# Kernel tuning notes

Measured on AMD Instinct MI355X. Metric: run time of the kernel, lower is better.

The kernel has to match this reference:

```python
import jax, jax.numpy as jnp
import numpy as np
import math

B, S, D = 1, 2048, 2048          # batch, seq_len, hidden_size
H, HD = 16, 128                  # attention heads, head_dim
HV, R, NV, K = 4, 128, 2048, 4   # inner value heads, retrieval dim, num_inner_values, values per head


def rotate_half(x):
    x1, x2 = x[..., :x.shape[-1] // 2], x[..., x.shape[-1] // 2:]
    return jnp.concatenate((-x2, x1), axis=-1)


def setup_inputs() -> dict:
    key = jax.random.key(0)
    ks = jax.random.split(key, 8)
    hidden_states = jax.random.normal(ks[0], (B, S, D), jnp.float32)
    attention_mask = jnp.ones((B, S), jnp.float32)
    # standard RoPE tables, shape [B, S, HD]
    inv_freq = 1.0 / (10000.0 ** (jnp.arange(0, HD, 2, dtype=jnp.float32) / HD))
    freqs = jnp.outer(jnp.arange(S, dtype=jnp.float32), inv_freq)
    emb = jnp.concatenate((freqs, freqs), axis=-1)
    cos = jnp.broadcast_to(jnp.cos(emb)[None], (B, S, HD))
    sin = jnp.broadcast_to(jnp.sin(emb)[None], (B, S, HD))
    # learned per-head dynamic mask (binary, like torch.round init)
    dynamic_mask = jnp.round(jax.random.uniform(ks[1], (H, S), jnp.float32))
    sc = 0.02
    Wq = jax.random.normal(ks[2], (D, D), jnp.float32) * sc
    Wk = jax.random.normal(ks[3], (D, D), jnp.float32) * sc
    Wvq = jax.random.normal(ks[4], (D, HV * R), jnp.float32) * sc
    v_keys = jax.random.normal(ks[5], (HV, R, NV), jnp.float32) * sc
    v_embed = jax.random.normal(ks[6], (NV, D), jnp.float32) * sc
    Wo = jax.random.normal(ks[7], (D, D), jnp.float32) * sc
    return dict(hidden_states=hidden_states, attention_mask=attention_mask,
                cos=cos, sin=sin, dynamic_mask=dynamic_mask,
                Wq=Wq, Wk=Wk, Wvq=Wvq, v_keys=v_keys, v_embed=v_embed, Wo=Wo)


def reference(hidden_states, attention_mask, cos, sin, dynamic_mask,
              Wq, Wk, Wvq, v_keys, v_embed, Wo):
    b, s, d = hidden_states.shape
    q = hidden_states @ Wq
    k = hidden_states @ Wk
    # ---- inner_func: product-key style value retrieval ----
    vq = (hidden_states @ Wvq).reshape(b, s, HV, R).transpose(0, 2, 1, 3)  # [b,HV,s,R]
    sim = jnp.einsum('bhsr,hrn->bhsn', vq, v_keys)                         # [b,HV,s,NV]
    _, idx = jax.lax.top_k(sim, K)                                         # [b,HV,s,K]
    ve = v_embed[idx]                                                      # [b,HV,s,K,d]
    v = hidden_states * ve.sum(axis=3).sum(axis=1)                         # [b,s,d]
    # ---- heads ----
    q = q.reshape(b, s, H, HD).transpose(0, 2, 1, 3)
    k = k.reshape(b, s, H, HD).transpose(0, 2, 1, 3)
    v = v.reshape(b, s, H, HD).transpose(0, 2, 1, 3)
    # NOTE: original code rotates ONLY q (k is never rotated) -- kept faithfully
    cu, su = cos[:, None], sin[:, None]                                    # [b,1,s,HD]
    q = q * cu + rotate_half(q) * su
    attn = jnp.einsum('bhqd,bhkd->bhqk', q, k) / math.sqrt(HD)
    # ---- causal mask fused with per-head dynamic mask ----
    min_v = jnp.finfo(attn.dtype).min
    i = jnp.arange(s)
    causal = jnp.where(i[None, :] > i[:, None], min_v, 0.0).astype(attn.dtype)   # [s,s]
    causal = jnp.broadcast_to(causal[None, None], (b, H, s, s))
    am = attention_mask[:, None, None, :] * dynamic_mask[None, :, None, :s]      # [b,H,1,s]
    mask = jnp.where(causal + am == 0, min_v, causal)
    p = jax.nn.softmax(attn + mask, axis=-1)
    out = jnp.einsum('bhqk,bhkd->bhqd', p, v)
    out = out.transpose(0, 2, 1, 3).reshape(b, s, d)
    return out @ Wo
```

## Files before the change

kernel.cpp:

```cpp
#include <hip/hip_runtime.h>
#include <float.h>

#define NEG_MIN (-3.4028234663852886e38f)
#define INV_SQRT_HD 0.08838834764831845f
#define SCALE_L2E 0.12751791437968458f

typedef __attribute__((ext_vector_type(8))) short bf16x8;
typedef __attribute__((ext_vector_type(8))) unsigned short u16x8;
typedef __attribute__((ext_vector_type(4))) float f32x4;

__device__ __forceinline__ void gload_lds16(const void* g, void* l) {
  __builtin_amdgcn_global_load_lds((const __attribute__((address_space(1))) void*)g,
                                   (__attribute__((address_space(3))) void*)l, 16, 0, 0);
}
__device__ __forceinline__ ushort f2bf(float x) {
  union { float f; unsigned u; } v; v.f = x;
  unsigned r = v.u + 0x7fffu + ((v.u >> 16) & 1u);
  return (ushort)(r >> 16);
}
__device__ __forceinline__ float bf2f(ushort u) {
  union { unsigned i; float f; } v; v.i = ((unsigned)u) << 16; return v.f;
}
template<int CTRL>
__device__ __forceinline__ float dpp_ror(float x) {
  return __int_as_float(__builtin_amdgcn_mov_dpp(__float_as_int(x), CTRL, 0xF, 0xF, true));
}
template<int CTRL>
__device__ __forceinline__ unsigned dpp_ror_u(unsigned x) {
  return (unsigned)__builtin_amdgcn_mov_dpp((int)x, CTRL, 0xF, 0xF, true);
}
__device__ __forceinline__ unsigned wave_umax64(unsigned x) {
  x = max(x, dpp_ror_u<0x121>(x));
  x = max(x, dpp_ror_u<0x122>(x));
  x = max(x, dpp_ror_u<0x124>(x));
  x = max(x, dpp_ror_u<0x128>(x));
  x = max(x, (unsigned)__shfl_xor((int)x, 16));
  x = max(x, (unsigned)__shfl_xor((int)x, 32));
  return x;
}
__device__ __forceinline__ unsigned bf_sortable(ushort b) {
  return (b & 0x8000u) ? (unsigned)(b ^ 0xFFFFu) : (unsigned)(b | 0x8000u);
}

__global__ __launch_bounds__(256) void gemm_f32_sk(
    const float* __restrict__ A, int lda,
    const float* __restrict__ B, int ldb,
    float* __restrict__ Cp, int ldc, int M, int N, int Kchunk)
{
  __shared__ float As[16][132];
  __shared__ float Bs[16][132];
  const int t = threadIdx.x, tx = t & 15, ty = t >> 4;
  const int bm = blockIdx.y << 7, bn = blockIdx.x << 7;
  const int k0base = blockIdx.z * Kchunk;
  const int arr = t >> 2, ac = (t & 3) << 2;
  const int brr = t >> 5, bc = (t & 31) << 2;

  float acc[8][8];
#pragma unroll
  for (int i = 0; i < 8; ++i)
#pragma unroll
    for (int j = 0; j < 8; ++j) acc[i][j] = 0.f;

  float4 pa0, pa1, pb0, pb1;
  pa0 = *(const float4*)(A + (size_t)(bm + arr) * lda + k0base + ac);
  pa1 = *(const float4*)(A + (size_t)(bm + arr + 64) * lda + k0base + ac);
  pb0 = *(const float4*)(B + (size_t)(k0base + brr) * ldb + bn + bc);
  pb1 = *(const float4*)(B + (size_t)(k0base + brr + 8) * ldb + bn + bc);

  for (int k0 = 0; k0 < Kchunk; k0 += 16) {
    __syncthreads();
    As[ac + 0][arr] = pa0.x; As[ac + 1][arr] = pa0.y;
    As[ac + 2][arr] = pa0.z; As[ac + 3][arr] = pa0.w;
    As[ac + 0][arr + 64] = pa1.x; As[ac + 1][arr + 64] = pa1.y;
    As[ac + 2][arr + 64] = pa1.z; As[ac + 3][arr + 64] = pa1.w;
    *(float4*)(&Bs[brr][bc])     = pb0;
    *(float4*)(&Bs[brr + 8][bc]) = pb1;
    __syncthreads();
    if (k0 + 16 < Kchunk) {
      int kn = k0base + k0 + 16;
      pa0 = *(const float4*)(A + (size_t)(bm + arr) * lda + kn + ac);
      pa1 = *(const float4*)(A + (size_t)(bm + arr + 64) * lda + kn + ac);
      pb0 = *(const float4*)(B + (size_t)(kn + brr) * ldb + bn + bc);
      pb1 = *(const float4*)(B + (size_t)(kn + brr + 8) * ldb + bn + bc);
    }
#pragma unroll
    for (int kk = 0; kk < 16; ++kk) {
      float4 a0 = *(const float4*)(&As[kk][ty * 8]);
      float4 a1 = *(const float4*)(&As[kk][ty * 8 + 4]);
      float4 b0 = *(const float4*)(&Bs[kk][tx * 4]);
      float4 b1 = *(const float4*)(&Bs[kk][tx * 4 + 64]);
      float av[8] = {a0.x, a0.y, a0.z, a0.w, a1.x, a1.y, a1.z, a1.w};
      float bv[8] = {b0.x, b0.y, b0.z, b0.w, b1.x, b1.y, b1.z, b1.w};
#pragma unroll
      for (int i = 0; i < 8; ++i)
#pragma unroll
        for (int j = 0; j < 8; ++j)
          acc[i][j] = fmaf(av[i], bv[j], acc[i][j]);
    }
  }
  float* C = Cp + (size_t)blockIdx.z * M * N;
#pragma unroll
  for (int i = 0; i < 8; ++i) {
    int row = bm + ty * 8 + i;
    *(float4*)(C + (size_t)row * ldc + bn + tx * 4) =
        make_float4(acc[i][0], acc[i][1], acc[i][2], acc[i][3]);
    *(float4*)(C + (size_t)row * ldc + bn + tx * 4 + 64) =
        make_float4(acc[i][4], acc[i][5], acc[i][6], acc[i][7]);
  }
}

__global__ __launch_bounds__(256) void reduce16_cvt(const float* __restrict__ Cp,
    float* __restrict__ vq, ushort* __restrict__ vq_bf)
{
  int i = (blockIdx.x * 256 + threadIdx.x) << 2;
  float4 s = make_float4(0.f, 0.f, 0.f, 0.f);
#pragma unroll
  for (int z = 0; z < 16; ++z) {
    float4 a = *(const float4*)(Cp + (size_t)z * 1048576 + i);
    s.x += a.x; s.y += a.y; s.z += a.z; s.w += a.w;
  }
  *(float4*)(vq + i) = s;
  ushort4 o; o.x = f2bf(s.x); o.y = f2bf(s.y); o.z = f2bf(s.z); o.w = f2bf(s.w);
  *(ushort4*)(vq_bf + i) = o;
}

template<int OUT_BF16, int ROPE>
__global__ __launch_bounds__(256) void gemm_bf16(
    const ushort* __restrict__ A0, int lda,
    const ushort* __restrict__ Bt0, int ldb,
    void* __restrict__ C0, int ldc, int Kd,
    size_t strA, size_t strB, size_t strC,
    const float* __restrict__ cosb, const float* __restrict__ sinb)
{
  const ushort* A  = A0  + blockIdx.z * strA;
  const ushort* Bt = Bt0 + blockIdx.z * strB;
  __shared__ ushort smem_g[2 * 128 * 64];
  ushort* As = smem_g;
  ushort* Bs = smem_g + 128 * 64;
  const int t = threadIdx.x, w = t >> 6, lane = t & 63;
  const int lr = lane & 15, lk = lane >> 4;
  const int bm = blockIdx.y << 7, bn = blockIdx.x << 7;
  const int wm = (w >> 1) << 6, wn = (w & 1) << 6;
  f32x4 acc[4][4];
#pragma unroll
  for (int i = 0; i < 4; ++i)
#pragma unroll
    for (int j = 0; j < 4; ++j) acc[i][j] = (f32x4){0.f, 0.f, 0.f, 0.f};

  for (int k0 = 0; k0 < Kd; k0 += 64) {
    __syncthreads();
#pragma unroll
    for (int qI = 0; qI < 4; ++qI) {
      int b = w * 4096 + qI * 1024 + lane * 16;
      int row = b >> 7, colb = b & 127;
      int src = colb ^ ((row & 7) << 4);
      gload_lds16((const char*)A + ((size_t)(bm + row) * lda + k0) * 2 + src,
                  (char*)As + w * 4096 + qI * 1024);
    }
#pragma unroll
    for (int qI = 0; qI < 4; ++qI) {
      int b = w * 4096 + qI * 1024 + lane * 16;
      int row = b >> 7, colb = b & 127;
      int src = colb ^ ((row & 7) << 4);
      gload_lds16((const char*)Bt + ((size_t)(bn + row) * ldb + k0) * 2 + src,
                  (char*)Bs + w * 4096 + qI * 1024);
    }
    __syncthreads();
#pragma unroll
    for (int kk = 0; kk < 2; ++kk) {
      bf16x8 af[4], bf[4];
#pragma unroll
      for (int mi = 0; mi < 4; ++mi) {
        int row = wm + mi * 16 + lr;
        af[mi] = *(const bf16x8*)((const char*)As + row * 128 + ((kk * 64 + lk * 16) ^ ((row & 7) << 4)));
      }
#pragma unroll
      for (int ni = 0; ni < 4; ++ni) {
        int row = wn + ni * 16 + lr;
        bf[ni] = *(const bf16x8*)((const char*)Bs + row * 128 + ((kk * 64 + lk * 16) ^ ((row & 7) << 4)));
      }
#pragma unroll
      for (int mi = 0; mi < 4; ++mi)
#pragma unroll
        for (int ni = 0; ni < 4; ++ni)
          acc[mi][ni] = __builtin_amdgcn_mfma_f32_16x16x32_bf16(af[mi], bf[ni], acc[mi][ni], 0, 0, 0);
    }
  }

  if (ROPE && blockIdx.x < 16) {
    __syncthreads();
    ushort* Pl = smem_g;
#pragma unroll
    for (int mi = 0; mi < 4; ++mi)
#pragma unroll
      for (int j = 0; j < 4; ++j) {
        int rl = wm + mi * 16 + lk * 4 + j;
#pragma unroll
        for (int ni = 0; ni < 4; ++ni)
          Pl[rl * 128 + wn + ni * 16 + lr] = f2bf(acc[mi][ni][j]);
      }
    __syncthreads();
    const bool lo = (wn == 0);
#pragma unroll
    for (int mi = 0; mi < 4; ++mi)
#pragma unroll
      for (int j = 0; j < 4; ++j) {
        int rl = wm + mi * 16 + lk * 4 + j;
        int row = bm + rl;
#pragma unroll
        for (int ni = 0; ni < 4; ++ni) {
          int d = wn + ni * 16 + lr;
          float a = bf2f(Pl[rl * 128 + d]);
          float b = bf2f(Pl[rl * 128 + (d ^ 64)]);
          float cs = cosb[row * 128 + d], sn = sinb[row * 128 + d];
          float v = lo ? (a * cs - b * sn) : (a * cs + b * sn);
          ((ushort*)C0)[(size_t)row * ldc + bn + d] = f2bf(v);
        }
      }
    return;
  }

#pragma unroll
  for (int mi = 0; mi < 4; ++mi)
#pragma unroll
    for (int j = 0; j < 4; ++j) {
      int row = bm + wm + mi * 16 + lk * 4 + j;
#pragma unroll
      for (int ni = 0; ni < 4; ++ni) {
        int col = bn + wn + ni * 16 + lr;
        if (OUT_BF16) ((ushort*)C0)[blockIdx.z * strC + (size_t)row * ldc + col] = f2bf(acc[mi][ni][j]);
        else          ((float*)C0)[blockIdx.z * strC + (size_t)row * ldc + col]  = acc[mi][ni][j];
      }
    }
}

__global__ __launch_bounds__(256) void transpose_cvt_vk(
    const float* __restrict__ src0, ushort* __restrict__ dstb,
    float* __restrict__ dstf)
{
  const float* src = src0 + (size_t)blockIdx.z * 262144;
  ushort* db = dstb + (size_t)blockIdx.z * 262144;
  float*  df = dstf + (size_t)blockIdx.z * 262144;
  __shared__ float tile[64][65];
  const int r0 = blockIdx.y << 6, c0 = blockIdx.x << 6;
  const int t = threadIdx.x;
  for (int i = t; i < 1024; i += 256) {
    int r = i >> 4, c = (i & 15) << 2;
    float4 v = *(const float4*)(src + (size_t)(r0 + r) * 2048 + c0 + c);
    tile[r][c] = v.x; tile[r][c+1] = v.y; tile[r][c+2] = v.z; tile[r][c+3] = v.w;
  }
  __syncthreads();
  int c = t >> 2, rb = (t & 3) << 4;
#pragma unroll
  for (int u = 0; u < 16; u += 4) {
    float4 f = make_float4(tile[rb+u+0][c], tile[rb+u+1][c],
                           tile[rb+u+2][c], tile[rb+u+3][c]);
    ushort4 o; o.x = f2bf(f.x); o.y = f2bf(f.y); o.z = f2bf(f.z); o.w = f2bf(f.w);
    *(ushort4*)(db + (size_t)(c0 + c) * 128 + r0 + rb + u) = o;
    *(float4*) (df + (size_t)(c0 + c) * 128 + r0 + rb + u) = f;
  }
}

__global__ __launch_bounds__(256) void transpose_cvt_w3(
    const float* __restrict__ srcA, const float* __restrict__ srcB,
    const float* __restrict__ srcC, ushort* __restrict__ dst0)
{
  const float* src = (blockIdx.z == 0) ? srcA : (blockIdx.z == 1) ? srcB : srcC;
  ushort* dst = dst0 + (size_t)blockIdx.z * 4194304;
  __shared__ float tile[64][65];
  const int r0 = blockIdx.y << 6, c0 = blockIdx.x << 6;
  const int t = threadIdx.x;
  for (int i = t; i < 1024; i += 256) {
    int r = i >> 4, c = (i & 15) << 2;
    float4 v = *(const float4*)(src + (size_t)(r0 + r) * 2048 + c0 + c);
    tile[r][c] = v.x; tile[r][c+1] = v.y; tile[r][c+2] = v.z; tile[r][c+3] = v.w;
  }
  __syncthreads();
  int c = t >> 2, rb = (t & 3) << 4;
#pragma unroll
  for (int u = 0; u < 16; u += 4) {
    ushort4 o;
    o.x = f2bf(tile[rb+u+0][c]); o.y = f2bf(tile[rb+u+1][c]);
    o.z = f2bf(tile[rb+u+2][c]); o.w = f2bf(tile[rb+u+3][c]);
    *(ushort4*)(dst + (size_t)(c0 + c) * 2048 + r0 + rb + u) = o;
  }
}

__global__ __launch_bounds__(256) void transpose_bf(
    const ushort* __restrict__ src, ushort* __restrict__ dst)
{
  __shared__ ushort tile[64][66];
  const int r0 = blockIdx.y << 6, c0 = blockIdx.x << 6;
  const int t = threadIdx.x;
  for (int i = t; i < 512; i += 256) {
    int r = i >> 3, c8 = (i & 7) << 3;
    *(u16x8*)(&tile[r][c8]) = *(const u16x8*)(src + (size_t)(r0 + r) * 2048 + c0 + c8);
  }
  __syncthreads();
  for (int i = t; i < 512; i += 256) {
    int c = i >> 3, r8 = (i & 7) << 3;
    u16x8 o;
#pragma unroll
    for (int u = 0; u < 8; ++u) o[u] = tile[r8 + u][c];
    *(u16x8*)(dst + (size_t)(c0 + c) * 2048 + r0 + r8) = o;
  }
}

__global__ __launch_bounds__(256) void cvt2_bf16(const float* __restrict__ srcA,
    ushort* __restrict__ dstA, const float* __restrict__ srcB,
    ushort* __restrict__ dstB)
{
  int gid = blockIdx.x * 256 + threadIdx.x;
  const float* s; ushort* d; int i;
  if (gid < 1048576) { s = srcA; d = dstA; i = gid; }
  else               { s = srcB; d = dstB; i = gid - 1048576; }
  float4 v = ((const float4*)s)[i];
  ushort4 o; o.x = f2bf(v.x); o.y = f2bf(v.y); o.z = f2bf(v.z); o.w = f2bf(v.w);
  ((ushort4*)d)[i] = o;
}

__global__ __launch_bounds__(256) void topk_sel(const ushort* __restrict__ sim,
    const float* __restrict__ vq, const float* __restrict__ vkTf,
    int* __restrict__ idxo)
{
  const int row = blockIdx.x * 4 + (threadIdx.x >> 6);
  const int hv = row >> 11, s = row & 2047;
  const int lane = threadIdx.x & 63;
  const ushort* r = sim + (size_t)row * 2048;

  unsigned v[8];
#pragma unroll
  for (int p = 0; p < 8; ++p) v[p] = 0u;
  for (int j = 0; j < 4; ++j) {
    int nb = (lane + (j << 6)) << 3;
    u16x8 e = *(const u16x8*)(r + nb);
#pragma unroll
    for (int u = 0; u < 8; ++u) {
      unsigned pk = (bf_sortable(e[u]) << 16) | (unsigned)(2047 - (nb + u));
      if (pk > v[7]) {
        v[7] = pk;
#pragma unroll
        for (int p = 7; p > 0; --p)
          if (v[p] > v[p-1]) { unsigned tt = v[p]; v[p] = v[p-1]; v[p-1] = tt; }
      }
    }
  }
  int out_n[8];
#pragma unroll
  for (int r8 = 0; r8 < 8; ++r8) {
    unsigned m = wave_umax64(v[0]);
    out_n[r8] = 2047 - (int)(m & 0x7FFu);
    if (v[0] == m) {
#pragma unroll
      for (int p = 0; p < 7; ++p) v[p] = v[p+1];
      v[7] = 0u;
    }
  }
  const int c = lane & 7, rc = lane >> 3;
  int n = 0;
#pragma unroll
  for (int p = 0; p < 8; ++p) if (p == c) n = out_n[p];
  const float* vqr = vq + (size_t)s * 512 + hv * 128 + rc * 16;
  const float* vkf = vkTf + (size_t)hv * 262144 + (size_t)n * 128 + rc * 16;
  float acc = 0.f;
#pragma unroll
  for (int u = 0; u < 16; ++u) acc = fmaf(vqr[u], vkf[u], acc);
  acc += __shfl_xor(acc, 8);
  acc += __shfl_xor(acc, 16);
  acc += __shfl_xor(acc, 32);
  float cv = acc; int ci = n;
  int picks[4];
#pragma unroll
  for (int p = 0; p < 4; ++p) {
    float bv = cv; int bi = ci;
#pragma unroll
    for (int d = 1; d < 8; d <<= 1) {
      float ov = __shfl_xor(bv, d); int oi = __shfl_xor(bi, d);
      if (ov > bv || (ov == bv && oi < bi)) { bv = ov; bi = oi; }
    }
    picks[p] = bi;
    if (bi == ci) cv = -FLT_MAX;
  }
  if (lane == 0) {
#pragma unroll
    for (int p = 0; p < 4; ++p) idxo[(size_t)row * 4 + p] = picks[p];
  }
}

__global__ __launch_bounds__(256) void gather_mul_bf(const float* __restrict__ hs,
    const ushort* __restrict__ vemb_bf, const int* __restrict__ idx,
    ushort* __restrict__ vb)
{
  const int s = blockIdx.x;
  const int t = threadIdx.x;
  __shared__ int id[16];
  if (t < 16) id[t] = idx[((size_t)(t >> 2) * 2048 + s) * 4 + (t & 3)];
  __syncthreads();
  int d0 = t << 3;
  float g[8] = {0.f, 0.f, 0.f, 0.f, 0.f, 0.f, 0.f, 0.f};
#pragma unroll
  for (int e = 0; e < 16; ++e) {
    u16x8 ve = *(const u16x8*)(vemb_bf + (size_t)id[e] * 2048 + d0);
#pragma unroll
    for (int u = 0; u < 8; ++u) g[u] += bf2f(ve[u]);
  }
  float4 h0 = *(const float4*)(hs + (size_t)s * 2048 + d0);
  float4 h1 = *(const float4*)(hs + (size_t)s * 2048 + d0 + 4);
  float hv[8] = {h0.x, h0.y, h0.z, h0.w, h1.x, h1.y, h1.z, h1.w};
  u16x8 o;
#pragma unroll
  for (int u = 0; u < 8; ++u) o[u] = f2bf(hv[u] * g[u]);
  *(u16x8*)(vb + (size_t)s * 2048 + d0) = o;
}

__global__ __launch_bounds__(256) void vmean_part(const ushort* __restrict__ vb,
                                                  float* __restrict__ part)
{
  const int h = blockIdx.y, chunk = blockIdx.x;
  const int t = threadIdx.x, d = t & 127, half = t >> 7;
  float s = 0.f;
  int r0 = chunk * 256 + half * 128;
  for (int r = r0; r < r0 + 128; ++r)
    s += bf2f(vb[(size_t)r * 2048 + h * 128 + d]);
  __shared__ float red[256];
  red[t] = s;
  __syncthreads();
  if (t < 128) part[(size_t)(h * 8 + chunk) * 128 + d] = red[t] + red[t + 128];
}

__global__ __launch_bounds__(256) void vmean_i0(const float* __restrict__ part,
    const float* __restrict__ amask, const float* __restrict__ dmask,
    float* __restrict__ vmean, int* __restrict__ i0)
{
  const int h = blockIdx.x, t = threadIdx.x;
  if (t < 128) {
    float s = 0.f;
#pragma unroll
    for (int c = 0; c < 8; ++c) s += part[(size_t)(h * 8 + c) * 128 + t];
    vmean[h * 128 + t] = s * (1.f / 2048.f);
  }
  int best = 0x7fffffff;
  for (int j = t; j < 2048; j += 256) {
    if (amask[j] * dmask[h * 2048 + j] != 0.f) { best = j; break; }
  }
  __shared__ int red[256];
  red[t] = best;
  __syncthreads();
  for (int off = 128; off > 0; off >>= 1) {
    if (t < off) red[t] = min(red[t], red[t + off]);
    __syncthreads();
  }
  if (t == 0) i0[h] = red[0];
}

#define QLD 4096
__global__ __launch_bounds__(512) void attn_mfma(
    const ushort* __restrict__ qb, const ushort* __restrict__ kb,
    const ushort* __restrict__ vt, const float* __restrict__ amask,
    const float* __restrict__ dmask, const float* __restrict__ vmean,
    const int* __restrict__ i0, ushort* __restrict__ ao)
{
  const int L  = blockIdx.x;
  const int pr = L >> 4;
  const int h  = (L & 7) | (((L >> 3) & 1) << 3);
  const int t  = threadIdx.x, w = t >> 6, lane = t & 63;
  const int g  = w >> 2, wg = w & 3;
  const int lr = lane & 15, lk = lane >> 4;

  __shared__ char smem[155648];
  float* accL  = (float*)smem;
  float* smv   = (float*)(smem + 33792);
  float* slv   = (float*)(smem + 33792 + 512);
  float* maddL = (float*)(smem + 147456);

  const int i0h = i0[h];

  for (int j = t; j < 2048; j += 512)
    maddL[j] = (amask[j] * dmask[h * 2048 + j] == 0.f) ? NEG_MIN : 0.f;

  for (int sp = 0; sp < 2; ++sp) {
    const int stripe = (sp == 0) ? pr : 31 - pr;
    const int q0 = stripe << 6;
    const int ntiles = stripe + 1;

    __syncthreads();

    const int qrow = q0 + wg * 16 + lr;
    bf16x8 qf[4];
#pragma unroll
    for (int kk = 0; kk < 4; ++kk)
      qf[kk] = *(const bf16x8*)(qb + (size_t)qrow * QLD + h * 128 + kk * 32 + lk * 8);

    if (g < ntiles) {
      const int c0 = g << 6;
#pragma unroll
      for (int qI = 0; qI < 4; ++qI) {
        int b = wg * 4096 + qI * 1024 + lane * 16;
        int row = b >> 8, colb = b & 255;
        int src = colb ^ ((row & 7) << 4);
        gload_lds16((const char*)kb + ((size_t)(c0 + row) * QLD + h * 128) * 2 + src,
                    smem + g * 32768 + b);
      }
#pragma unroll
      for (int qI = 0; qI < 4; ++qI) {
        int b = wg * 4096 + qI * 1024 + lane * 16;
        int row = b >> 7, colb = b & 127;
        int src = colb ^ ((row & 7) << 4);
        gload_lds16((const char*)vt + ((size_t)(h * 128 + row) * 2048 + c0) * 2 + src,
                    smem + 65536 + g * 32768 + b);
      }
    }

    float m[4], l[4];
    f32x4 acc_o[8];
#pragma unroll
    for (int j = 0; j < 4; ++j) { m[j] = -FLT_MAX; l[j] = 0.f; }
#pragma unroll
    for (int ni = 0; ni < 8; ++ni) acc_o[ni] = (f32x4){0.f, 0.f, 0.f, 0.f};

    int cur = 0;
    const int niter = (ntiles + 1) >> 1;
    for (int it = 0; it < niter; ++it) {
      const int tile = 2 * it + g;
      const int c0 = tile << 6;
      __syncthreads();

      float madd[4];
      if (tile < ntiles) {
#pragma unroll
        for (int ni = 0; ni < 4; ++ni)
          madd[ni] = maddL[c0 + ni * 16 + lr];
      }

      if (tile + 2 < ntiles) {
        const int cn = c0 + 128;
        const int nb = cur ^ 1;
#pragma unroll
        for (int qI = 0; qI < 4; ++qI) {
          int b = wg * 4096 + qI * 1024 + lane * 16;
          int row = b >> 8, colb = b & 255;
          int src = colb ^ ((row & 7) << 4);
          gload_lds16((const char*)kb + ((size_t)(cn + row) * QLD + h * 128) * 2 + src,
                      smem + g * 32768 + nb * 16384 + b);
        }
#pragma unroll
        for (int qI = 0; qI < 4; ++qI) {
          int b = wg * 4096 + qI * 1024 + lane * 16;
          int row = b >> 7, colb = b & 127;
          int src = colb ^ ((row & 7) << 4);
          gload_lds16((const char*)vt + ((size_t)(h * 128 + row) * 2048 + cn) * 2 + src,
                      smem + 65536 + g * 32768 + nb * 16384 + b);
        }
      }

      if (tile < ntiles) {
        const bool diag = (tile == stripe);
        const char* Kbase = smem + g * 32768 + cur * 16384;
        const char* Vbase = smem + 65536 + g * 32768 + cur * 16384;
        char* Pbase = smem + 131072 + g * 8192;

        f32x4 sacc[4];
#pragma unroll
        for (int ni = 0; ni < 4; ++ni) sacc[ni] = (f32x4){0.f, 0.f, 0.f, 0.f};
        __builtin_amdgcn_s_setprio(1);
#pragma unroll
        for (int kk = 0; kk < 4; ++kk) {
#pragma unroll
          for (int ni = 0; ni < 4; ++ni) {
            int krow = ni * 16 + lr;
            bf16x8 bfr = *(const bf16x8*)(Kbase + krow * 256 + ((kk * 64 + lk * 16) ^ ((krow & 7) << 4)));
            sacc[ni] = __builtin_amdgcn_mfma_f32_16x16x32_bf16(qf[kk], bfr, sacc[ni], 0, 0, 0);
          }
        }
        __builtin_amdgcn_s_setprio(0);

#pragma unroll
        for (int j = 0; j < 4; ++j) {
          int grow = q0 + wg * 16 + lk * 4 + j;
          float x[4]; float tmax = -FLT_MAX;
#pragma unroll
          for (int ni = 0; ni < 4; ++ni) {
            float v = fmaf(sacc[ni][j], SCALE_L2E, madd[ni]);
            if (diag && c0 + ni * 16 + lr > grow) v = NEG_MIN;
            x[ni] = v; tmax = fmaxf(tmax, v);
          }
          tmax = fmaxf(tmax, dpp_ror<0x121>(tmax));
          tmax = fmaxf(tmax, dpp_ror<0x122>(tmax));
          tmax = fmaxf(tmax, dpp_ror<0x124>(tmax));
          tmax = fmaxf(tmax, dpp_ror<0x128>(tmax));
          float mn = fmaxf(m[j], tmax);
          float psum = 0.f;
          int prow = wg * 16 + lk * 4 + j;
#pragma unroll
          for (int ni = 0; ni < 4; ++ni) {
            float p = exp2f(x[ni] - mn);
            psum += p;
            *(ushort*)(Pbase + prow * 128 + ((2 * (ni * 16 + lr)) ^ ((prow & 7) << 4))) = f2bf(p);
          }
          psum += dpp_ror<0x121>(psum);
          psum += dpp_ror<0x122>(psum);
          psum += dpp_ror<0x124>(psum);
          psum += dpp_ror<0x128>(psum);
          if (mn > m[j]) {
            float sc = exp2f(m[j] - mn);
            l[j] *= sc;
#pragma unroll
            for (int ni = 0; ni < 8; ++ni) acc_o[ni][j] *= sc;
            m[j] = mn;
          }
          l[j] += psum;
        }

        __builtin_amdgcn_s_setprio(1);
#pragma unroll
        for (int kk = 0; kk < 2; ++kk) {
          int prow = wg * 16 + lr;
          bf16x8 a = *(const bf16x8*)(Pbase + prow * 128 + ((kk * 64 + lk * 16) ^ ((prow & 7) << 4)));
#pragma unroll
          for (int ni = 0; ni < 8; ++ni) {
            int vrow = ni * 16 + lr;
            bf16x8 bfr = *(const bf16x8*)(Vbase + vrow * 128 + ((kk * 64 + lk * 16) ^ ((vrow & 7) << 4)));
            acc_o[ni] = __builtin_amdgcn_mfma_f32_16x16x32_bf16(a, bfr, acc_o[ni], 0, 0, 0);
          }
        }
        __builtin_amdgcn_s_setprio(0);
      }
      cur ^= 1;
    }

    __syncthreads();
    if (lr == 0) {
#pragma unroll
      for (int j = 0; j < 4; ++j) {
        int r = wg * 16 + lk * 4 + j;
        smv[g * 64 + r] = m[j];
        slv[g * 64 + r] = l[j];
      }
    }
    __syncthreads();
    float myf[4], lcomb[4];
#pragma unroll
    for (int j = 0; j < 4; ++j) {
      int r = wg * 16 + lk * 4 + j;
      float m0 = smv[r], m1 = smv[64 + r];
      float l0 = slv[r], l1 = slv[64 + r];
      float mm = fmaxf(m0, m1);
      float f0 = exp2f(m0 - mm), f1 = exp2f(m1 - mm);
      lcomb[j] = l0 * f0 + l1 * f1;
      myf[j] = (g == 0) ? f0 : f1;
    }
    if (g == 1) {
#pragma unroll
      for (int j = 0; j < 4; ++j) {
        int r = wg * 16 + lk * 4 + j;
#pragma unroll
        for (int ni = 0; ni < 8; ++ni)
          accL[r * 132 + ni * 16 + lr] = acc_o[ni][j] * myf[j];
      }
    }
    __syncthreads();
    if (g == 0) {
#pragma unroll
      for (int j = 0; j < 4; ++j) {
        int row = q0 + wg * 16 + lk * 4 + j;
        int r = wg * 16 + lk * 4 + j;
        if (row < i0h) {
#pragma unroll
          for (int ni = 0; ni < 8; ++ni)
            ao[(size_t)row * 2048 + h * 128 + ni * 16 + lr] = f2bf(vmean[h * 128 + ni * 16 + lr]);
        } else {
          float inv = 1.f / lcomb[j];
#pragma unroll
          for (int ni = 0; ni < 8; ++ni) {
            float o = fmaf(acc_o[ni][j], myf[j], accL[r * 132 + ni * 16 + lr]);
            ao[(size_t)row * 2048 + h * 128 + ni * 16 + lr] = f2bf(o * inv);
          }
        }
      }
    }
  }
}

extern "C" void kernel_launch(void* const* d_in, const int* in_sizes, int n_in,
                              void* d_out, int out_size, void* d_ws, size_t ws_size,
                              hipStream_t stream)
{
  const float* hs    = (const float*)d_in[0];
  const float* amask = (const float*)d_in[1];
  const float* cosb  = (const float*)d_in[2];
  const float* sinb  = (const float*)d_in[3];
  const float* dmask = (const float*)d_in[4];
  const float* Wq    = (const float*)d_in[5];
  const float* Wk    = (const float*)d_in[6];
  const float* Wvq   = (const float*)d_in[7];
  const float* vkeys = (const float*)d_in[8];
  const float* vemb  = (const float*)d_in[9];
  const float* Wo    = (const float*)d_in[10];
  float* outp = (float*)d_out;

  char* ws = (char*)d_ws;
  const size_t MB = 1048576;
  float*  pvq     = (float*) (ws + 0);
  float*  vq_f32  = (float*) (ws + 64*MB);
  ushort* vq_bf   = (ushort*)(ws + 68*MB);
  ushort* vkT     = (ushort*)(ws + 0);
  ushort* sim_bf  = (ushort*)(ws + 2*MB);
  int*    idx     = (int*)   (ws + 34*MB);
  float*  vkTf32  = (float*) (ws + 36*MB);
  ushort* vemb_bf = (ushort*)(ws + 35*MB);
  ushort* hs_bf   = (ushort*)(ws + 43*MB);
  ushort* vb      = (ushort*)(ws + 0);
  ushort* vt      = (ushort*)(ws + 8*MB);
  float*  part    = (float*) (ws + 51*MB);
  float*  vmean   = (float*) (ws + 51*MB + 65536);
  int*    i0b     = (int*)   (ws + 51*MB + 73728);
  ushort* WBig    = (ushort*)(ws + 16*MB);
  ushort* WoT     = (ushort*)(ws + 32*MB);
  ushort* qkC     = (ushort*)(ws + 52*MB);
  ushort* ao      = (ushort*)(ws + 0);

  dim3 blk(256);
  gemm_f32_sk<<<dim3(4, 16, 16), blk, 0, stream>>>(hs, 2048, Wvq, 512, pvq, 512, 2048, 512, 128);
  reduce16_cvt<<<dim3(1024), blk, 0, stream>>>(pvq, vq_f32, vq_bf);
  transpose_cvt_vk<<<dim3(32, 2, 4), blk, 0, stream>>>(vkeys, vkT, vkTf32);
  gemm_bf16<1, 0><<<dim3(16, 16, 4), blk, 0, stream>>>(vq_bf, 512, vkT, 128,
      sim_bf, 2048, 128, 128, 262144, 4194304, nullptr, nullptr);
  topk_sel<<<dim3(2048), blk, 0, stream>>>(sim_bf, vq_f32, vkTf32, idx);
  cvt2_bf16<<<dim3(8192), blk, 0, stream>>>(vemb, vemb_bf, hs, hs_bf);
  gather_mul_bf<<<dim3(2048), blk, 0, stream>>>(hs, vemb_bf, idx, vb);
  transpose_bf<<<dim3(32, 32), blk, 0, stream>>>(vb, vt);
  vmean_part<<<dim3(8, 16), blk, 0, stream>>>(vb, part);
  vmean_i0<<<dim3(16), blk, 0, stream>>>(part, amask, dmask, vmean, i0b);
  transpose_cvt_w3<<<dim3(32, 32, 3), blk, 0, stream>>>(Wq, Wk, Wo, WBig);
  gemm_bf16<1, 1><<<dim3(32, 16, 1), blk, 0, stream>>>(hs_bf, 2048, WBig, 2048,
      qkC, 4096, 2048, 0, 0, 0, cosb, sinb);
  attn_mfma<<<dim3(256), dim3(512), 0, stream>>>(qkC, qkC + 2048, vt, amask, dmask, vmean, i0b, ao);
  gemm_bf16<0, 0><<<dim3(16, 16, 1), blk, 0, stream>>>(ao, 2048, WoT, 2048,
      outp, 2048, 2048, 0, 0, 0, nullptr, nullptr);
}
```

Baseline: 337.5 us.

## Compute softmax row sums via MFMA with ones and lazily rescale running max

Replaces the per-row DPP reduction of the softmax denominator with an extra MFMA of the bf16 P tile against a ones vector, accumulating the row sum in a matrix accumulator. It also skips the max reduction and rescale when every lane's partial max stays within a threshold (16 in log2 units) of the running max, so stale maxima are tolerated. This removes cross-lane shuffle and ALU work from the softmax inner loop. In exchange it adds one MFMA per k-step, computes the row sum from bf16-rounded probabilities, and allows exponentials up to 2^16, which could affect precision.

```diff
diff --git a/kernel.cpp b/kernel.cpp
--- a/kernel.cpp
+++ b/kernel.cpp
@@ -475,6 +475,10 @@
 
   const int i0h = i0[h];
 
+  bf16x8 onesb;
+#pragma unroll
+  for (int u = 0; u < 8; ++u) onesb[u] = (short)0x3F80;
+
   for (int j = t; j < 2048; j += 512)
     maddL[j] = (amask[j] * dmask[h * 2048 + j] == 0.f) ? NEG_MIN : 0.f;
 
@@ -511,10 +515,11 @@
       }
     }
 
-    float m[4], l[4];
+    float m[4];
+    f32x4 acc_l = (f32x4){0.f, 0.f, 0.f, 0.f};
     f32x4 acc_o[8];
 #pragma unroll
-    for (int j = 0; j < 4; ++j) { m[j] = -FLT_MAX; l[j] = 0.f; }
+    for (int j = 0; j < 4; ++j) m[j] = -FLT_MAX;
 #pragma unroll
     for (int ni = 0; ni < 8; ++ni) acc_o[ni] = (f32x4){0.f, 0.f, 0.f, 0.f};
 
@@ -577,38 +582,35 @@
 #pragma unroll
         for (int j = 0; j < 4; ++j) {
           int grow = q0 + wg * 16 + lk * 4 + j;
-          float x[4]; float tmax = -FLT_MAX;
+          float x[4];
 #pragma unroll
           for (int ni = 0; ni < 4; ++ni) {
             float v = fmaf(sacc[ni][j], SCALE_L2E, madd[ni]);
             if (diag && c0 + ni * 16 + lr > grow) v = NEG_MIN;
-            x[ni] = v; tmax = fmaxf(tmax, v);
+            x[ni] = v;
           }
-          tmax = fmaxf(tmax, dpp_ror<0x121>(tmax));
-          tmax = fmaxf(tmax, dpp_ror<0x122>(tmax));
-          tmax = fmaxf(tmax, dpp_ror<0x124>(tmax));
-          tmax = fmaxf(tmax, dpp_ror<0x128>(tmax));
-          float mn = fmaxf(m[j], tmax);
-          float psum = 0.f;
+          float pm = fmaxf(fmaxf(x[0], x[1]), fmaxf(x[2], x[3]));
+          if (!__all(pm <= m[j] + 16.f)) {
+            float tmax = pm;
+            tmax = fmaxf(tmax, dpp_ror<0x121>(tmax));
+            tmax = fmaxf(tmax, dpp_ror<0x122>(tmax));
+            tmax = fmaxf(tmax, dpp_ror<0x124>(tmax));
+            tmax = fmaxf(tmax, dpp_ror<0x128>(tmax));
+            float mn = fmaxf(m[j], tmax);
+            if (mn > m[j]) {
+              float sc = exp2f(m[j] - mn);
+              acc_l[j] *= sc;
+#pragma unroll
+              for (int ni = 0; ni < 8; ++ni) acc_o[ni][j] *= sc;
+              m[j] = mn;
+            }
+          }
           int prow = wg * 16 + lk * 4 + j;
 #pragma unroll
           for (int ni = 0; ni < 4; ++ni) {
-            float p = exp2f(x[ni] - mn);
-            psum += p;
+            float p = exp2f(x[ni] - m[j]);
             *(ushort*)(Pbase + prow * 128 + ((2 * (ni * 16 + lr)) ^ ((prow & 7) << 4))) = f2bf(p);
           }
-          psum += dpp_ror<0x121>(psum);
-          psum += dpp_ror<0x122>(psum);
-          psum += dpp_ror<0x124>(psum);
-          psum += dpp_ror<0x128>(psum);
-          if (mn > m[j]) {
-            float sc = exp2f(m[j] - mn);
-            l[j] *= sc;
-#pragma unroll
-            for (int ni = 0; ni < 8; ++ni) acc_o[ni][j] *= sc;
-            m[j] = mn;
-          }
-          l[j] += psum;
         }
 
         __builtin_amdgcn_s_setprio(1);
@@ -616,6 +618,7 @@
         for (int kk = 0; kk < 2; ++kk) {
           int prow = wg * 16 + lr;
           bf16x8 a = *(const bf16x8*)(Pbase + prow * 128 + ((kk * 64 + lk * 16) ^ ((prow & 7) << 4)));
+          acc_l = __builtin_amdgcn_mfma_f32_16x16x32_bf16(a, onesb, acc_l, 0, 0, 0);
 #pragma unroll
           for (int ni = 0; ni < 8; ++ni) {
             int vrow = ni * 16 + lr;
@@ -634,7 +637,7 @@
       for (int j = 0; j < 4; ++j) {
         int r = wg * 16 + lk * 4 + j;
         smv[g * 64 + r] = m[j];
-        slv[g * 64 + r] = l[j];
+        slv[g * 64 + r] = acc_l[j];
       }
     }
     __syncthreads();
```

Measured after the change: 326.0 us. 1.04x faster.
